# Kernel tuning notes

Hardware: AMD Instinct MI355X
Metric: run time of the kernel (lower is better)

## Reference

```python
import jax, jax.numpy as jnp
import numpy as np

N = 8_388_608        # cohort size (2^23)
T_MAX = 1_000_000    # distinct time values -> ~8 ties per unique time


def setup_inputs() -> dict:
    key = jax.random.key(0)
    k1, k2, k3 = jax.random.split(key, 3)
    x = jax.random.normal(k1, (N,), dtype=jnp.float32)  # risk scores
    times = jax.random.randint(k2, (N,), 0, T_MAX).astype(jnp.float32)
    events = (jax.random.uniform(k3, (N,)) < 0.7).astype(jnp.float32)
    target = jnp.stack([times, events], axis=1)  # [N, 2] = [time, event]
    return {"input": x, "target": target}


def _cox_breslow_sqrt_loss(x, target):
    times = target[:, 0]
    events_all = target[:, 1]
    n = x.shape[0]
    # Sort by descending time (risk set = prefix in this ordering).
    sort_idx = jnp.argsort(-times)
    t = times[sort_idx]
    ev = events_all[sort_idx]
    xs = x[sort_idx]
    # Stable prefix log-sum-exp over the risk set.
    log_cum = jax.lax.cumlogsumexp(xs)
    # end_idx[i] = last index of the tie group containing i (groups are
    # contiguous after sorting). Reverse running-min over positions of
    # group-last elements.
    is_last = jnp.concatenate([t[:-1] != t[1:], jnp.ones((1,), dtype=bool)])
    pos = jnp.where(is_last, jnp.arange(n), n)
    end_idx = jnp.flip(jax.lax.cummin(jnp.flip(pos)))
    # Breslow: -sum(x*ev) + sum_groups logcum[group_end] * (#events in group)
    #        == -sum((x - logcum[end_idx]) * ev)
    loss = -jnp.sum((xs - log_cum[end_idx]) * ev)
    # reduction='mean' -> sqrt(loss / n)
    return jnp.sqrt(loss / n)


def reference(input, target):
    return _cox_breslow_sqrt_loss(input, target)
```

## Files before the change

### kernel.cpp

```cpp
#include <hip/hip_runtime.h>
#include <math.h>

#define TMAX 1000000
#define BINW 4096
#define BINSHIFT 12
#define NBIN 245
#define PADN (NBIN * BINW)
#define TILE 8192
#define NTHR 512
#define CAP 36864
#define CURSOR_STRIDE 16
#define BT_STRIDE 8
#define FIXSCALE 65536.0f
#define INV_FIXSCALE (1.0 / 65536.0)

#define OFF_SCAL     0
#define OFF_DONE     16
#define OFF_CURSOR   64
#define OFF_BINTOT   15744
#define OFF_PAYLOAD  31488
#define MEMSET_BYTES 31424
#define NEED_FULL    ((size_t)OFF_PAYLOAD + (size_t)NBIN * CAP * 4)
#define FB_BINTOT    15744
#define FB_CEXCL     17792
#define FB_BEXP      31488
#define FB_BEV       (FB_BEXP + PADN * 4)
#define NEED_MIN     ((size_t)FB_BEV + PADN * 4)

__device__ __forceinline__ int clamp_tau(float t) {
    int tau = (int)t;
    if (tau < 0) tau = 0;
    if (tau >= TMAX) tau = TMAX - 1;
    return tau;
}

__device__ __forceinline__ unsigned enc_payload(float xv, float tv, float ev_f, int* bin_out) {
    int tau = clamp_tau(tv);
    *bin_out = tau >> BINSHIFT;
    int fine = tau & (BINW - 1);
    float ex = __expf(xv);
    unsigned bb = __float_as_uint(ex);
    bb = (bb + 0x7FFFu + ((bb >> 16) & 1u)) >> 16;
    unsigned ev = (ev_f != 0.0f) ? 1u : 0u;
    return (bb << 16) | ((unsigned)fine << 1) | ev;
}

__device__ __forceinline__ float dec_exp(unsigned p) {
    return __uint_as_float((p >> 16) << 16);
}

__device__ __forceinline__ void hist1(unsigned long long* hist, unsigned p) {
    float ex = dec_exp(p);
    unsigned fx = __float2uint_rn(ex * FIXSCALE);
    unsigned long long add = ((unsigned long long)(p & 1u) << 48) | (unsigned long long)fx;
    atomicAdd(&hist[(p >> 1) & (BINW - 1)], add);
}

__device__ __forceinline__ void hist4(unsigned long long* hist, uint4 pv) {
    hist1(hist, pv.x); hist1(hist, pv.y); hist1(hist, pv.z); hist1(hist, pv.w);
}

__global__ __launch_bounds__(NTHR) void k_scatter(const float* __restrict__ x,
                                                  const float* __restrict__ tgt,
                                                  unsigned* __restrict__ cursor,
                                                  unsigned* __restrict__ payload,
                                                  double* __restrict__ bintot,
                                                  double* __restrict__ evx_out, int n) {
    __shared__ unsigned cnt[256];
    __shared__ unsigned lpre[256];
    __shared__ unsigned base_s[256];
    __shared__ unsigned pay_lds[TILE];
    __shared__ unsigned char binof[TILE];
    __shared__ unsigned wtot_s[8];
    __shared__ double wpart[8];
    const int t = threadIdx.x;
    const int lane = t & 63;
    const int wv = t >> 6;
    if (t < 256) cnt[t] = 0;
    __syncthreads();

    const int tile0 = blockIdx.x * TILE;
    const int tilecount = min(TILE, n - tile0);
    unsigned pay[16], meta[16];
    double evx = 0.0;

    if (tilecount == TILE) {
        const float4* x4 = (const float4*)x;
        const float4* t4 = (const float4*)tgt;
        const int g0 = blockIdx.x * (TILE / 4);
#pragma unroll
        for (int j = 0; j < 4; ++j) {
            const int g = g0 + j * NTHR + t;
            float4 xv = x4[g];
            float4 ta = t4[2 * g];
            float4 tb = t4[2 * g + 1];
            float xs[4] = {xv.x, xv.y, xv.z, xv.w};
            float ts[4] = {ta.x, ta.z, tb.x, tb.z};
            float es[4] = {ta.y, ta.w, tb.y, tb.w};
#pragma unroll
            for (int e = 0; e < 4; ++e) {
                int bin;
                unsigned p = enc_payload(xs[e], ts[e], es[e], &bin);
                unsigned r = atomicAdd(&cnt[bin], 1u);
                pay[4 * j + e] = p;
                meta[4 * j + e] = ((unsigned)bin << 13) | r;
                if (p & 1) evx += (double)xs[e];
            }
        }
    } else {
        const float2* tg2 = (const float2*)tgt;
#pragma unroll
        for (int j = 0; j < 16; ++j) {
            int idx = tile0 + j * NTHR + t;
            if (idx < n) {
                float xv = x[idx];
                float2 te = tg2[idx];
                int bin;
                unsigned p = enc_payload(xv, te.x, te.y, &bin);
                unsigned r = atomicAdd(&cnt[bin], 1u);
                pay[j] = p;
                meta[j] = ((unsigned)bin << 13) | r;
                if (p & 1) evx += (double)xv;
            } else {
                meta[j] = 0xFFFFFFFFu;
            }
        }
    }
    __syncthreads();

    const unsigned c = (t < 256) ? cnt[t] : 0u;
    unsigned pfx = c;
#pragma unroll
    for (int d = 1; d < 64; d <<= 1) {
        unsigned u = __shfl_up(pfx, d);
        if (lane >= d) pfx += u;
    }
    if (lane == 63) wtot_s[wv] = pfx;
    __syncthreads();
    unsigned wbase = 0;
    if (t < 256) {
        for (int w = 0; w < wv; ++w) wbase += wtot_s[w];
    }
    const unsigned excl = (t < 256) ? (wbase + pfx - c) : 0u;
    if (t < 256) lpre[t] = excl;

    if (t < NBIN && c) base_s[t] = atomicAdd(&cursor[t * CURSOR_STRIDE], c);

    if (t < NBIN) {
        for (unsigned k = excl; k < excl + c; ++k) binof[k] = (unsigned char)t;
    }
    __syncthreads();

#pragma unroll
    for (int j = 0; j < 16; ++j) {
        if (meta[j] != 0xFFFFFFFFu) {
            unsigned bin = meta[j] >> 13;
            pay_lds[lpre[bin] + (meta[j] & 0x1FFFu)] = pay[j];
        }
    }
    __syncthreads();

    if (t < NBIN && c) {
        float s = 0.0f;
        for (unsigned k = excl; k < excl + c; ++k) s += dec_exp(pay_lds[k]);
        unsafeAtomicAdd(&bintot[t * BT_STRIDE], (double)s);
    }

    if (tilecount == TILE) {
#pragma unroll 4
        for (int kk = 0; kk < TILE / NTHR; ++kk) {
            const int k = kk * NTHR + t;
            unsigned b = binof[k];
            unsigned pos = base_s[b] + ((unsigned)k - lpre[b]);
            if (pos < CAP) payload[(size_t)b * CAP + pos] = pay_lds[k];
        }
    } else {
        for (int k = t; k < tilecount; k += NTHR) {
            unsigned b = binof[k];
            unsigned pos = base_s[b] + ((unsigned)k - lpre[b]);
            if (pos < CAP) payload[(size_t)b * CAP + pos] = pay_lds[k];
        }
    }

#pragma unroll
    for (int d = 32; d > 0; d >>= 1) {
        double u = __shfl_down(evx, d);
        if (lane + d < 64) evx += u;
    }
    if (lane == 0) wpart[wv] = evx;
    __syncthreads();
    if (t == 0) {
        double s = 0.0;
        for (int w = 0; w < 8; ++w) s += wpart[w];
        atomicAdd(evx_out, s);
    }
}

__global__ __launch_bounds__(1024) void k_fused(const unsigned* __restrict__ payload,
                                                const unsigned* __restrict__ cursor,
                                                const double* __restrict__ bintot,
                                                double* __restrict__ scal,
                                                unsigned* __restrict__ done,
                                                float* __restrict__ out, int n) {
    __shared__ unsigned long long hist[BINW];
    __shared__ double wsumA[16];
    __shared__ double wsum[16];
    __shared__ double bcast;
    const int b = blockIdx.x;
    const int t = threadIdx.x;
    const int lane = t & 63;
    const int wv = t >> 6;

#pragma unroll
    for (int j = 0; j < BINW / 1024; ++j) hist[t + j * 1024] = 0ull;
    __syncthreads();

    unsigned cnt = cursor[b * CURSOR_STRIDE];
    if (cnt > CAP) cnt = CAP;
    const unsigned* seg = payload + (size_t)b * CAP;
    const uint4* seg4 = (const uint4*)seg;
    const unsigned n4 = cnt >> 2;
    unsigned i = t;
    for (; i + 1024 < n4; i += 2048) {
        uint4 a = seg4[i];
        uint4 c4 = seg4[i + 1024];
        hist4(hist, a);
        hist4(hist, c4);
    }
    for (; i < n4; i += 1024) hist4(hist, seg4[i]);
    for (unsigned k = (n4 << 2) + t; k < cnt; k += 1024) hist1(hist, seg[k]);
    __syncthreads();

    double ce = 0.0;
    for (int idx = b + 1 + t; idx < NBIN; idx += 1024) ce += bintot[idx * BT_STRIDE];
#pragma unroll
    for (int d = 32; d > 0; d >>= 1) {
        double u = __shfl_down(ce, d);
        if (lane + d < 64) ce += u;
    }
    if (lane == 0) wsumA[wv] = ce;
    __syncthreads();
    if (t == 0) {
        double s = 0.0;
        for (int w = 0; w < 16; ++w) s += wsumA[w];
        bcast = s;
    }
    __syncthreads();
    const double cexcl = bcast;

    const int tb = t * 4;
    double vex[4];
    unsigned vcnt[4];
    double segtot = 0.0;
#pragma unroll
    for (int j = 0; j < 4; ++j) {
        unsigned long long h = hist[tb + j];
        vex[j] = (double)(h & 0xFFFFFFFFFFFFull) * INV_FIXSCALE;
        vcnt[j] = (unsigned)(h >> 48);
        segtot += vex[j];
    }
    double isuf = segtot;
#pragma unroll
    for (int d = 1; d < 64; d <<= 1) {
        double u = __shfl_down(isuf, d);
        if (lane + d < 64) isuf += u;
    }
    if (lane == 0) wsum[wv] = isuf;
    __syncthreads();
    double wexcl = 0.0;
    for (int w = wv + 1; w < 16; ++w) wexcl += wsum[w];

    double run = cexcl + wexcl + (isuf - segtot);
    double local = 0.0;
#pragma unroll
    for (int j = 3; j >= 0; --j) {
        run += vex[j];
        if (vcnt[j]) local += (double)vcnt[j] * log(run);
    }

#pragma unroll
    for (int d = 32; d > 0; d >>= 1) {
        double u = __shfl_down(local, d);
        if (lane + d < 64) local += u;
    }
    if (lane == 0) wsumA[wv] = local;
    __syncthreads();
    if (t == 0) {
        double s = 0.0;
        for (int w = 0; w < 16; ++w) s += wsumA[w];
        unsafeAtomicAdd(&scal[1], s);
        __threadfence();
        unsigned tk = atomicAdd(done, 1u);
        if (tk == NBIN - 1) {
            double ld = unsafeAtomicAdd(&scal[1], 0.0);
            double loss = ld - scal[0];
            if (loss < 0.0) loss = 0.0;
            out[0] = (float)sqrt(loss / (double)n);
        }
    }
}

__global__ void k_accum(const float* __restrict__ x, const float* __restrict__ tgt,
                        float* __restrict__ bexp, float* __restrict__ bev,
                        double* __restrict__ evx_out, int ngroups) {
    double local = 0.0;
    const int nt = gridDim.x * blockDim.x;
    const int tid = blockIdx.x * blockDim.x + threadIdx.x;
    const float4* x4 = (const float4*)x;
    const float4* t4 = (const float4*)tgt;
    for (int g = tid; g < ngroups; g += nt) {
        float4 xv = x4[g];
        float4 ta = t4[2 * g];
        float4 tb = t4[2 * g + 1];
        float xs[4] = {xv.x, xv.y, xv.z, xv.w};
        float ts[4] = {ta.x, ta.z, tb.x, tb.z};
        float es[4] = {ta.y, ta.w, tb.y, tb.w};
#pragma unroll
        for (int j = 0; j < 4; ++j) {
            int tau = clamp_tau(ts[j]);
            unsafeAtomicAdd(&bexp[tau], __expf(xs[j]));
            if (es[j] != 0.0f) unsafeAtomicAdd(&bev[tau], es[j]);
            local += (double)(es[j] * xs[j]);
        }
    }
    __shared__ double sm[256];
    sm[threadIdx.x] = local;
    __syncthreads();
    for (int s = 128; s > 0; s >>= 1) {
        if (threadIdx.x < s) sm[threadIdx.x] += sm[threadIdx.x + s];
        __syncthreads();
    }
    if (threadIdx.x == 0) atomicAdd(evx_out, sm[0]);
}

__global__ void k_chunksum(const float* __restrict__ bexp, double* __restrict__ bintot) {
    const int b = blockIdx.x;
    double local = 0.0;
    for (int i = b * BINW + (int)threadIdx.x; i < (b + 1) * BINW; i += (int)blockDim.x)
        local += (double)bexp[i];
    __shared__ double sm[256];
    sm[threadIdx.x] = local;
    __syncthreads();
    for (int s = 128; s > 0; s >>= 1) {
        if (threadIdx.x < s) sm[threadIdx.x] += sm[threadIdx.x + s];
        __syncthreads();
    }
    if (threadIdx.x == 0) bintot[b] = sm[0];
}

__global__ __launch_bounds__(256) void k_scanbins(const double* __restrict__ bintot,
                                                  double* __restrict__ cexcl) {
    __shared__ double sm[256];
    const int t = threadIdx.x;
    sm[t] = (t < NBIN) ? bintot[t] : 0.0;
    __syncthreads();
    for (int d = 1; d < 256; d <<= 1) {
        double v = (t + d < 256) ? sm[t + d] : 0.0;
        __syncthreads();
        sm[t] += v;
        __syncthreads();
    }
    double e = (t + 1 < 256) ? sm[t + 1] : 0.0;
    __syncthreads();
    cexcl[t] = e;
}

__global__ __launch_bounds__(256) void k_logdot_g(const float* __restrict__ bexp,
                                                  const float* __restrict__ bev,
                                                  const double* __restrict__ cexcl,
                                                  double* __restrict__ logdot) {
    const int b = blockIdx.x;
    const int t = threadIdx.x;
    const float4* e4 = (const float4*)(bexp + b * BINW + t * 16);
    const float4* v4 = (const float4*)(bev + b * BINW + t * 16);
    float ve[16], vv[16];
#pragma unroll
    for (int q = 0; q < 4; ++q) {
        float4 a = e4[q], bb = v4[q];
        ve[4 * q] = a.x; ve[4 * q + 1] = a.y; ve[4 * q + 2] = a.z; ve[4 * q + 3] = a.w;
        vv[4 * q] = bb.x; vv[4 * q + 1] = bb.y; vv[4 * q + 2] = bb.z; vv[4 * q + 3] = bb.w;
    }
    double segtot = 0.0;
#pragma unroll
    for (int j = 0; j < 16; ++j) segtot += (double)ve[j];
    __shared__ double sm[256];
    sm[t] = segtot;
    __syncthreads();
    for (int d = 1; d < 256; d <<= 1) {
        double v = (t + d < 256) ? sm[t + d] : 0.0;
        __syncthreads();
        sm[t] += v;
        __syncthreads();
    }
    double excl = (t < 255) ? sm[t + 1] : 0.0;
    double run = cexcl[b] + excl;
    double local = 0.0;
#pragma unroll
    for (int j = 15; j >= 0; --j) {
        run += (double)ve[j];
        if (vv[j] > 0.0f) local += (double)vv[j] * log(run);
    }
    __syncthreads();
    sm[t] = local;
    __syncthreads();
    for (int s = 128; s > 0; s >>= 1) {
        if (t < s) sm[t] += sm[t + s];
        __syncthreads();
    }
    if (t == 0) atomicAdd(logdot, sm[0]);
}

__global__ void k_final(const double* __restrict__ scal, float* __restrict__ out, int n) {
    if (threadIdx.x == 0 && blockIdx.x == 0) {
        double loss = scal[1] - scal[0];
        if (loss < 0.0) loss = 0.0;
        out[0] = (float)sqrt(loss / (double)n);
    }
}

extern "C" void kernel_launch(void* const* d_in, const int* in_sizes, int n_in,
                              void* d_out, int out_size, void* d_ws, size_t ws_size,
                              hipStream_t stream) {
    const float* x = (const float*)d_in[0];
    const float* tgt = (const float*)d_in[1];
    float* out = (float*)d_out;
    int n = in_sizes[0];

    char* ws = (char*)d_ws;
    double* scal = (double*)(ws + OFF_SCAL);
    unsigned* done = (unsigned*)(ws + OFF_DONE);
    unsigned* cursor = (unsigned*)(ws + OFF_CURSOR);
    double* bintot = (double*)(ws + OFF_BINTOT);
    unsigned* payload = (unsigned*)(ws + OFF_PAYLOAD);

    if (ws_size >= NEED_FULL) {
        hipMemsetAsync(ws, 0, MEMSET_BYTES, stream);
        const int nblk = (n + TILE - 1) / TILE;
        k_scatter<<<nblk, NTHR, 0, stream>>>(x, tgt, cursor, payload, bintot, scal, n);
        k_fused<<<NBIN, 1024, 0, stream>>>(payload, cursor, bintot, scal, done, out, n);
    } else if (ws_size >= NEED_MIN) {
        float* bexp = (float*)(ws + FB_BEXP);
        float* bev = (float*)(ws + FB_BEV);
        double* bintotF = (double*)(ws + FB_BINTOT);
        double* cexclF = (double*)(ws + FB_CEXCL);
        hipMemsetAsync(ws, 0, NEED_MIN, stream);
        k_accum<<<2048, 256, 0, stream>>>(x, tgt, bexp, bev, scal, n / 4);
        k_chunksum<<<NBIN, 256, 0, stream>>>(bexp, bintotF);
        k_scanbins<<<1, 256, 0, stream>>>(bintotF, cexclF);
        k_logdot_g<<<NBIN, 256, 0, stream>>>(bexp, bev, cexclF, scal + 1);
        k_final<<<1, 1, 0, stream>>>(scal, out, n);
    }
}
```

Before: 166.4 us.

## Write scatter payload per bin with wave-parallel loops and fused bin sums

Replaces the per-element binof lookup and the serial per-thread bin exp-sum with a loop where each wavefront handles bins, lanes stride over the bin's elements, write the payload and accumulate exp sums, then reduce via shuffles. This removes the binof LDS array, its serial fill loop, and the serial per-bin summation done by single threads. In exchange, bins with ~33 elements use only part of a 64-lane wave, so lane utilisation in the write loop drops and each wave processes about 31 bins sequentially.

```diff
diff --git a/kernel.cpp b/kernel.cpp
--- a/kernel.cpp
+++ b/kernel.cpp
@@ -70,7 +70,6 @@
     __shared__ unsigned lpre[256];
     __shared__ unsigned base_s[256];
     __shared__ unsigned pay_lds[TILE];
-    __shared__ unsigned char binof[TILE];
     __shared__ unsigned wtot_s[8];
     __shared__ double wpart[8];
     const int t = threadIdx.x;
@@ -145,10 +144,6 @@
     if (t < 256) lpre[t] = excl;
 
     if (t < NBIN && c) base_s[t] = atomicAdd(&cursor[t * CURSOR_STRIDE], c);
-
-    if (t < NBIN) {
-        for (unsigned k = excl; k < excl + c; ++k) binof[k] = (unsigned char)t;
-    }
     __syncthreads();
 
 #pragma unroll
@@ -160,26 +155,21 @@
     }
     __syncthreads();
 
-    if (t < NBIN && c) {
-        float s = 0.0f;
-        for (unsigned k = excl; k < excl + c; ++k) s += dec_exp(pay_lds[k]);
-        unsafeAtomicAdd(&bintot[t * BT_STRIDE], (double)s);
-    }
-
-    if (tilecount == TILE) {
-#pragma unroll 4
-        for (int kk = 0; kk < TILE / NTHR; ++kk) {
-            const int k = kk * NTHR + t;
-            unsigned b = binof[k];
-            unsigned pos = base_s[b] + ((unsigned)k - lpre[b]);
-            if (pos < CAP) payload[(size_t)b * CAP + pos] = pay_lds[k];
-        }
-    } else {
-        for (int k = t; k < tilecount; k += NTHR) {
-            unsigned b = binof[k];
-            unsigned pos = base_s[b] + ((unsigned)k - lpre[b]);
-            if (pos < CAP) payload[(size_t)b * CAP + pos] = pay_lds[k];
-        }
+    for (int bin = wv; bin < NBIN; bin += 8) {
+        unsigned cb = cnt[bin];
+        if (!cb) continue;
+        unsigned base = base_s[bin];
+        unsigned ex0 = lpre[bin];
+        float vsum = 0.0f;
+        for (unsigned ofs = lane; ofs < cb; ofs += 64) {
+            unsigned val = pay_lds[ex0 + ofs];
+            unsigned pos = base + ofs;
+            if (pos < CAP) payload[(size_t)bin * CAP + pos] = val;
+            vsum += dec_exp(val);
+        }
+#pragma unroll
+        for (int d = 32; d > 0; d >>= 1) vsum += __shfl_down(vsum, d);
+        if (lane == 0) unsafeAtomicAdd(&bintot[bin * BT_STRIDE], (double)vsum);
     }
 
 #pragma unroll
```

New measurement: 179.8 us. +8.1%, slower.
